# Kernel optimization log

Measured on AMD Instinct MI355X. Metric: run time of the kernel, lower is better.

The kernel has to match this reference:

```python
import jax, jax.numpy as jnp
import numpy as np

N = 100000
E = 1600000
F_IN = 512
HID = 8
HEADS = 8
NUM_CLASSES = 40
NEG_SLOPE = 0.2


def setup_inputs() -> dict:
    key = jax.random.key(0)
    ks = jax.random.split(key, 12)
    x = jax.random.normal(ks[0], (N, F_IN), dtype=jnp.float32)
    edge_index = jax.random.randint(ks[1], (2, E), 0, N, dtype=jnp.int64)
    s1 = 1.0 / np.sqrt(F_IN)
    s2 = 1.0 / np.sqrt(HID * HEADS)
    W1 = jax.random.normal(ks[2], (F_IN, HEADS * HID), dtype=jnp.float32) * s1
    a_src1 = jax.random.normal(ks[3], (HEADS, HID), dtype=jnp.float32) * s1
    a_dst1 = jax.random.normal(ks[4], (HEADS, HID), dtype=jnp.float32) * s1
    b1 = jnp.zeros((HEADS * HID,), dtype=jnp.float32)
    W2 = jax.random.normal(ks[5], (HEADS * HID, NUM_CLASSES), dtype=jnp.float32) * s2
    a_src2 = jax.random.normal(ks[6], (1, NUM_CLASSES), dtype=jnp.float32) * s2
    a_dst2 = jax.random.normal(ks[7], (1, NUM_CLASSES), dtype=jnp.float32) * s2
    b2 = jnp.zeros((NUM_CLASSES,), dtype=jnp.float32)
    return {"x": x, "edge_index": edge_index, "W1": W1, "a_src1": a_src1,
            "a_dst1": a_dst1, "b1": b1, "W2": W2, "a_src2": a_src2,
            "a_dst2": a_dst2, "b2": b2}


def _gat_conv(x, src, dst, W, a_src, a_dst, b, heads, out_ch):
    # linear projection, per-head: [N, heads, out_ch]
    h = (x @ W).reshape(N, heads, out_ch)
    # per-node attention logits [N, heads]
    al_s = jnp.einsum('nhf,hf->nh', h, a_src)
    al_d = jnp.einsum('nhf,hf->nh', h, a_dst)
    # per-edge raw scores [E', heads]
    e = jax.nn.leaky_relu(al_s[src] + al_d[dst], NEG_SLOPE)
    # segment softmax over edges sharing a destination node
    m = jax.lax.stop_gradient(jax.ops.segment_max(e, dst, num_segments=N))
    m = jnp.where(jnp.isfinite(m), m, 0.0)
    e = jnp.exp(e - m[dst])
    denom = jax.ops.segment_sum(e, dst, num_segments=N)
    alpha = e / denom[dst]  # [E', heads]
    # scatter-weighted aggregation of gathered source features
    out = jax.ops.segment_sum(alpha[:, :, None] * h[src], dst, num_segments=N)
    return out.reshape(N, heads * out_ch) + b


def reference(x, edge_index, W1, a_src1, a_dst1, b1, W2, a_src2, a_dst2, b2):
    # PyG GATConv default: add self-loops
    loops = jnp.arange(N, dtype=edge_index.dtype)
    src = jnp.concatenate([edge_index[0], loops])
    dst = jnp.concatenate([edge_index[1], loops])
    h = _gat_conv(x, src, dst, W1, a_src1, a_dst1, b1, HEADS, HID)
    h = jax.nn.elu(h)
    # dropout(p=0.6) is identity in eval mode
    out = _gat_conv(h, src, dst, W2, a_src2, a_dst2, b2, 1, NUM_CLASSES)
    return jax.nn.log_softmax(out, axis=1)
```

## Files before the change

kernel.cpp:

```cpp
#include <hip/hip_runtime.h>
#include <hip/hip_bf16.h>
#include <cstdint>
#include <cstddef>

#define N_NODES 100000
#define N_EDGES 1600000
#define E_TOT   (N_EDGES + N_NODES)
#define F_IN    512
#define HEADS   8
#define HID     8
#define F_H     64
#define NC      40
#define NEG     0.2f

#define BSH    8
#define NB     391
#define CHUNKH 8192
#define NBH    ((E_TOT + CHUNKH - 1) / CHUNKH)
#define CHUNKF 8192
#define NBF    ((E_TOT + CHUNKF - 1) / CHUNKF)
#define CAP    7168
#define GEMM_G ((N_NODES + 63) / 64)

typedef __attribute__((ext_vector_type(8))) __bf16 bf16x8;
typedef __attribute__((ext_vector_type(4))) float f32x4;
typedef __attribute__((ext_vector_type(8))) unsigned short u16x8;

__device__ __forceinline__ float bf2f(unsigned short u) {
  unsigned int w = ((unsigned int)u) << 16;
  return __builtin_bit_cast(float, w);
}
__device__ __forceinline__ unsigned short f2bf(float f) {
  __hip_bfloat16 b = __float2bfloat16(f);
  return __builtin_bit_cast(unsigned short, b);
}
__device__ __forceinline__ float lrexp(float v) {
  v = (v > 0.f) ? v : NEG * v;
  return __expf(v);
}

__device__ __forceinline__ bool detect_i64(const int* __restrict__ ei) {
  int lane = threadIdx.x & 63;
  int v = ei[2 * lane + 1];
  return __ballot(v != 0) == 0ull;
}

__device__ __forceinline__ int load_dst(const int* __restrict__ ei, bool f, int i) {
  if (i < N_EDGES) return f ? ei[2 * (N_EDGES + i)] : ei[N_EDGES + i];
  return i - N_EDGES;
}
__device__ __forceinline__ int load_src(const int* __restrict__ ei, bool f, int i) {
  if (i < N_EDGES) return f ? ei[2 * i] : ei[i];
  return i - N_EDGES;
}

__global__ __launch_bounds__(256) void k_hist_pack(
    const int* __restrict__ ei, const float* __restrict__ W1,
    uint4* __restrict__ w1f, int* __restrict__ bcnt) {
  __shared__ int h[NB];
  const int t = threadIdx.x;
  if (blockIdx.x < 16) {
    int tid = blockIdx.x * 256 + t;
    int lane = tid & 63;
    int tt = (tid >> 6) & 3;
    int s = tid >> 8;
    int k0 = s * 32 + ((lane >> 4) << 3);
    int col = tt * 16 + (lane & 15);
    u16x8 v;
#pragma unroll
    for (int i = 0; i < 8; ++i) v[i] = f2bf(W1[(size_t)(k0 + i) * F_H + col]);
    w1f[tid] = __builtin_bit_cast(uint4, v);
    return;
  }
  const int blk = blockIdx.x - 16;
  const bool f = detect_i64(ei);
  for (int i = t; i < NB; i += 256) h[i] = 0;
  __syncthreads();
  const int base = blk * CHUNKH;
#pragma unroll
  for (int j = 0; j < CHUNKH / 256; ++j) {
    int i = base + t + j * 256;
    if (i < E_TOT) atomicAdd(&h[load_dst(ei, f, i) >> BSH], 1);
  }
  __syncthreads();
  for (int i = t; i < NB; i += 256)
    if (h[i]) atomicAdd(&bcnt[i], h[i]);
}

__global__ __launch_bounds__(512) void k_bscan(const int* __restrict__ bcnt,
                                               int* __restrict__ bstart,
                                               int* __restrict__ bcur,
                                               int* __restrict__ rowstart) {
  __shared__ int sh[512];
  const int t = threadIdx.x;
  int v = (t < NB) ? bcnt[t] : 0;
  sh[t] = v;
  __syncthreads();
  for (int d = 1; d < 512; d <<= 1) {
    int u = (t >= d) ? sh[t - d] : 0;
    __syncthreads();
    sh[t] += u;
    __syncthreads();
  }
  if (t < NB) {
    int e = sh[t] - v;
    bstart[t] = e;
    bcur[t] = e;
  }
  if (t == 0) { bstart[NB] = E_TOT; rowstart[N_NODES] = E_TOT; }
}

__global__ __launch_bounds__(256) void k_bfill(const int* __restrict__ ei,
                                               int* __restrict__ bcur,
                                               unsigned int* __restrict__ inter) {
  __shared__ unsigned int ent[CHUNKF];
  __shared__ int h[NB], ofs[NB], cur[NB], gpos[NB];
  const int t = threadIdx.x;
  const int base = blockIdx.x * CHUNKF;
  const bool f = detect_i64(ei);
  for (int i = t; i < NB; i += 256) h[i] = 0;
  __syncthreads();
#pragma unroll
  for (int j = 0; j < CHUNKF / 256; ++j) {
    int i = base + t + j * 256;
    if (i < E_TOT) atomicAdd(&h[load_dst(ei, f, i) >> BSH], 1);
  }
  __syncthreads();
  if (t < 64) {
    int loc[7];
    int s = 0;
#pragma unroll
    for (int k = 0; k < 7; ++k) {
      int ix = t * 7 + k;
      int hv = (ix < NB) ? h[ix] : 0;
      loc[k] = s;
      s += hv;
    }
    int incl = s;
    for (int dd = 1; dd < 64; dd <<= 1) {
      int u = __shfl_up(incl, dd);
      if (t >= dd) incl += u;
    }
    int excl = incl - s;
#pragma unroll
    for (int k = 0; k < 7; ++k) {
      int ix = t * 7 + k;
      if (ix < NB) ofs[ix] = excl + loc[k];
    }
  }
  __syncthreads();
  for (int i = t; i < NB; i += 256) {
    cur[i] = ofs[i];
    gpos[i] = h[i] ? atomicAdd(&bcur[i], h[i]) : 0;
  }
  __syncthreads();
#pragma unroll
  for (int j = 0; j < CHUNKF / 256; ++j) {
    int i = base + t + j * 256;
    if (i < E_TOT) {
      int s = load_src(ei, f, i);
      int d = load_dst(ei, f, i);
      int p = atomicAdd(&cur[d >> BSH], 1);
      ent[p] = ((unsigned int)(d & 255) << 24) | (unsigned int)s;
    }
  }
  __syncthreads();
  const int wv = t >> 6, ln = t & 63;
  for (int b = wv; b < NB; b += 4) {
    int c = h[b];
    if (!c) continue;
    int g = gpos[b], o = ofs[b];
    for (int i = ln; i < c; i += 64) inter[g + i] = ent[o + i];
  }
}

__global__ __launch_bounds__(256) void k_gemm1g(
    const float* __restrict__ x, const uint4* __restrict__ w1f,
    const float* __restrict__ a_src, const float* __restrict__ a_dst,
    unsigned short* __restrict__ h1b, float* __restrict__ als,
    float* __restrict__ ald) {
  __shared__ float xs[2 * 64 * 64];
  const int t = threadIdx.x;
  const int lane = t & 63;
  const int wv = t >> 6;
  const int rb = blockIdx.x * 64;

  const int srow_in_kb = lane >> 4;
  const int sc16 = lane & 15;

  const int myrow = wv * 16 + (lane & 15);
  const int m7 = myrow & 7;
  const int rowbase = myrow * 64;
  const int cg2 = (lane >> 4) << 1;

  f32x4 acc[4];
#pragma unroll
  for (int i = 0; i < 4; ++i) acc[i] = (f32x4){0.f, 0.f, 0.f, 0.f};

  auto STAGE = [&](int buf, int p) {
#pragma unroll
    for (int j = 0; j < 4; ++j) {
      int kb = wv * 4 + j;
      int r = kb * 4 + srow_in_kb;
      int gr = rb + r;
      if (gr >= N_NODES) gr = N_NODES - 1;
      int c16s = sc16 ^ (r & 7);
      const float* src = x + (size_t)gr * F_IN + p * 64 + c16s * 4;
      char* dst = (char*)xs + buf * 16384 + kb * 1024;
      __builtin_amdgcn_global_load_lds(
          (const __attribute__((address_space(1))) void*)src,
          (__attribute__((address_space(3))) void*)dst, 16, 0, 0);
    }
  };

  STAGE(0, 0);
  __syncthreads();
  int buf = 0;
#pragma unroll
  for (int p = 0; p < 8; ++p) {
    if (p < 7) STAGE(buf ^ 1, p + 1);
    const float* bufp = xs + buf * 4096;
#pragma unroll
    for (int s2 = 0; s2 < 2; ++s2) {
      const int sg = p * 2 + s2;
      const int c16a = s2 * 8 + cg2;
      float4 a0 = *reinterpret_cast<const float4*>(&bufp[rowbase + ((c16a ^ m7) << 2)]);
      float4 a1 = *reinterpret_cast<const float4*>(&bufp[rowbase + (((c16a + 1) ^ m7) << 2)]);
      uint4 b0 = w1f[(sg * 4 + 0) * 64 + lane];
      uint4 b1 = w1f[(sg * 4 + 1) * 64 + lane];
      uint4 b2 = w1f[(sg * 4 + 2) * 64 + lane];
      uint4 b3 = w1f[(sg * 4 + 3) * 64 + lane];
      bf16x8 af;
      af[0] = (__bf16)a0.x; af[1] = (__bf16)a0.y;
      af[2] = (__bf16)a0.z; af[3] = (__bf16)a0.w;
      af[4] = (__bf16)a1.x; af[5] = (__bf16)a1.y;
      af[6] = (__bf16)a1.z; af[7] = (__bf16)a1.w;
      acc[0] = __builtin_amdgcn_mfma_f32_16x16x32_bf16(af, __builtin_bit_cast(bf16x8, b0), acc[0], 0, 0, 0);
      acc[1] = __builtin_amdgcn_mfma_f32_16x16x32_bf16(af, __builtin_bit_cast(bf16x8, b1), acc[1], 0, 0, 0);
      acc[2] = __builtin_amdgcn_mfma_f32_16x16x32_bf16(af, __builtin_bit_cast(bf16x8, b2), acc[2], 0, 0, 0);
      acc[3] = __builtin_amdgcn_mfma_f32_16x16x32_bf16(af, __builtin_bit_cast(bf16x8, b3), acc[3], 0, 0, 0);
    }
    __syncthreads();
    buf ^= 1;
  }

  const int r0 = rb + wv * 16 + ((lane >> 4) << 2);
  const int c = lane & 15;
#pragma unroll
  for (int tt = 0; tt < 4; ++tt) {
#pragma unroll
    for (int i = 0; i < 4; ++i) {
      int r = r0 + i;
      if (r < N_NODES) h1b[(size_t)r * F_H + tt * 16 + c] = f2bf(acc[tt][i]);
    }
  }

  float asw[4], adw[4];
#pragma unroll
  for (int tt = 0; tt < 4; ++tt) {
    asw[tt] = a_src[tt * 16 + c];
    adw[tt] = a_dst[tt * 16 + c];
  }
  float sp[4][4], dp[4][4];
#pragma unroll
  for (int tt = 0; tt < 4; ++tt)
#pragma unroll
    for (int i = 0; i < 4; ++i) {
      sp[tt][i] = acc[tt][i] * asw[tt];
      dp[tt][i] = acc[tt][i] * adw[tt];
    }
#pragma unroll
  for (int dd = 1; dd < 8; dd <<= 1)
#pragma unroll
    for (int tt = 0; tt < 4; ++tt)
#pragma unroll
      for (int i = 0; i < 4; ++i) {
        sp[tt][i] += __shfl_xor(sp[tt][i], dd);
        dp[tt][i] += __shfl_xor(dp[tt][i], dd);
      }
  if ((c & 7) == 0) {
    const int hb = c >> 3;
#pragma unroll
    for (int i = 0; i < 4; ++i) {
      int r = r0 + i;
      if (r < N_NODES) {
#pragma unroll
        for (int tt = 0; tt < 4; ++tt) {
          als[(size_t)r * HEADS + tt * 2 + hb] = sp[tt][i];
          ald[(size_t)r * HEADS + tt * 2 + hb] = dp[tt][i];
        }
      }
    }
  }
}

__global__ __launch_bounds__(256) void k_cfill(const unsigned int* __restrict__ inter,
                                               const int* __restrict__ bstart,
                                               int* __restrict__ rowstart,
                                               int* __restrict__ csrc) {
  __shared__ unsigned int out_l[CAP];
  __shared__ int cnt[256], sc[256], cur2[256];
  const int t = threadIdx.x;
  const int b = blockIdx.x;
  const int segStart = bstart[b];
  const int L = bstart[b + 1] - segStart;
  cnt[t] = 0;
  __syncthreads();
  for (int i = t; i < L; i += 256) atomicAdd(&cnt[inter[segStart + i] >> 24], 1);
  __syncthreads();
  sc[t] = cnt[t];
  __syncthreads();
  for (int d = 1; d < 256; d <<= 1) {
    int v = (t >= d) ? sc[t - d] : 0;
    __syncthreads();
    sc[t] += v;
    __syncthreads();
  }
  const int excl = sc[t] - cnt[t];
  cur2[t] = excl;
  const int node = (b << BSH) + t;
  if (node < N_NODES) rowstart[node] = segStart + excl;
  __syncthreads();
  if (L <= CAP) {
    for (int i = t; i < L; i += 256) {
      unsigned int e = inter[segStart + i];
      int p = atomicAdd(&cur2[e >> 24], 1);
      out_l[p] = e & 0xFFFFFFu;
    }
    __syncthreads();
    for (int i = t; i < L; i += 256) csrc[segStart + i] = (int)out_l[i];
  } else {
    for (int i = t; i < L; i += 256) {
      unsigned int e = inter[segStart + i];
      int p = atomicAdd(&cur2[e >> 24], 1);
      csrc[segStart + p] = (int)(e & 0xFFFFFFu);
    }
  }
}

__global__ __launch_bounds__(256) void k_agg1n(
    const int* __restrict__ rowstart, const int* __restrict__ csrc,
    const unsigned short* __restrict__ h1b, const float* __restrict__ als,
    const float* __restrict__ ald, const float* __restrict__ b1,
    unsigned short* __restrict__ hactb) {
  const int w = (int)((blockIdx.x * 256 + threadIdx.x) >> 6);
  const int lane = threadIdx.x & 63;
  const int grp = lane >> 3;
  const int l = lane & 7;
  const int n = w * 8 + grp;
  const bool live = (n < N_NODES);
  const int e0 = live ? rowstart[n] : 0;
  const int e1 = live ? rowstart[n + 1] : 0;
  const float aldv = live ? ald[(size_t)n * HEADS + l] : 0.f;

  float den = 0.f;
  float acc[8];
#pragma unroll
  for (int k = 0; k < 8; ++k) acc[k] = 0.f;

  int e = e0;
  for (; e + 4 <= e1; e += 4) {
    int4 sv = *reinterpret_cast<const int4*>(&csrc[e]);
    float a0 = als[(size_t)sv.x * HEADS + l];
    float a1 = als[(size_t)sv.y * HEADS + l];
    float a2 = als[(size_t)sv.z * HEADS + l];
    float a3 = als[(size_t)sv.w * HEADS + l];
    uint4 u0 = *reinterpret_cast<const uint4*>(&h1b[(size_t)sv.x * F_H + l * 8]);
    uint4 u1 = *reinterpret_cast<const uint4*>(&h1b[(size_t)sv.y * F_H + l * 8]);
    uint4 u2 = *reinterpret_cast<const uint4*>(&h1b[(size_t)sv.z * F_H + l * 8]);
    uint4 u3 = *reinterpret_cast<const uint4*>(&h1b[(size_t)sv.w * F_H + l * 8]);
    float p0 = lrexp(a0 + aldv), p1 = lrexp(a1 + aldv);
    float p2 = lrexp(a2 + aldv), p3 = lrexp(a3 + aldv);
    den += (p0 + p1) + (p2 + p3);
    const unsigned int* q0 = &u0.x;
    const unsigned int* q1 = &u1.x;
    const unsigned int* q2 = &u2.x;
    const unsigned int* q3 = &u3.x;
#pragma unroll
    for (int k = 0; k < 4; ++k) {
      acc[2 * k]     += p0 * bf2f((unsigned short)q0[k]) + p1 * bf2f((unsigned short)q1[k])
                      + p2 * bf2f((unsigned short)q2[k]) + p3 * bf2f((unsigned short)q3[k]);
      acc[2 * k + 1] += p0 * bf2f((unsigned short)(q0[k] >> 16)) + p1 * bf2f((unsigned short)(q1[k] >> 16))
                      + p2 * bf2f((unsigned short)(q2[k] >> 16)) + p3 * bf2f((unsigned short)(q3[k] >> 16));
    }
  }
  for (; e < e1; ++e) {
    int s = csrc[e];
    float a = als[(size_t)s * HEADS + l];
    uint4 u = *reinterpret_cast<const uint4*>(&h1b[(size_t)s * F_H + l * 8]);
    float p = lrexp(a + aldv);
    den += p;
    const unsigned int* q = &u.x;
#pragma unroll
    for (int k = 0; k < 4; ++k) {
      acc[2 * k]     += p * bf2f((unsigned short)q[k]);
      acc[2 * k + 1] += p * bf2f((unsigned short)(q[k] >> 16));
    }
  }

  if (live) {
    float inv = 1.f / den;
    uint4 outw;
    unsigned int* ow = &outw.x;
#pragma unroll
    for (int k = 0; k < 4; ++k) {
      float ox = acc[2 * k] * inv + b1[l * 8 + 2 * k];
      float oy = acc[2 * k + 1] * inv + b1[l * 8 + 2 * k + 1];
      ox = (ox > 0.f) ? ox : expm1f(ox);
      oy = (oy > 0.f) ? oy : expm1f(oy);
      ow[k] = ((unsigned int)f2bf(oy) << 16) | (unsigned int)f2bf(ox);
    }
    *reinterpret_cast<uint4*>(&hactb[(size_t)n * F_H + l * 8]) = outw;
  }
}

__global__ __launch_bounds__(256) void k_l2proj(
    const unsigned short* __restrict__ hactb, const float* __restrict__ W2,
    const float* __restrict__ a_src2, const float* __restrict__ a_dst2,
    unsigned short* __restrict__ h2b, float* __restrict__ als2,
    float* __restrict__ ald2) {
  __shared__ float hs[64 * 68];
  __shared__ float w2s[F_H * NC];
  const int t = threadIdx.x;
  const int nb = blockIdx.x * 64;
  {
    int r0 = t >> 3, c8 = t & 7;
#pragma unroll
    for (int i = 0; i < 2; ++i) {
      int r = r0 + i * 32;
      int gr = nb + r;
      u16x8 v = (u16x8)(0);
      if (gr < N_NODES)
        v = *reinterpret_cast<const u16x8*>(&hactb[(size_t)gr * F_H + c8 * 8]);
#pragma unroll
      for (int k = 0; k < 8; ++k) hs[r * 68 + c8 * 8 + k] = bf2f(v[k]);
    }
  }
  for (int i = t; i < F_H * NC; i += 256) w2s[i] = W2[i];
  __syncthreads();

  const int node = t >> 2, cg = t & 3;
  float acc[10];
#pragma unroll
  for (int c = 0; c < 10; ++c) acc[c] = 0.f;
  for (int k = 0; k < F_H; ++k) {
    float xv = hs[node * 68 + k];
#pragma unroll
    for (int c = 0; c < 10; ++c) acc[c] += xv * w2s[k * NC + cg * 10 + c];
  }
  const int gn = nb + node;
  float ps = 0.f, pd = 0.f;
#pragma unroll
  for (int c = 0; c < 10; ++c) {
    ps += acc[c] * a_src2[cg * 10 + c];
    pd += acc[c] * a_dst2[cg * 10 + c];
  }
  ps += __shfl_xor(ps, 1); ps += __shfl_xor(ps, 2);
  pd += __shfl_xor(pd, 1); pd += __shfl_xor(pd, 2);
  if (gn < N_NODES) {
#pragma unroll
    for (int c = 0; c < 10; ++c) h2b[(size_t)gn * NC + cg * 10 + c] = f2bf(acc[c]);
    if (cg == 0) { als2[gn] = ps; ald2[gn] = pd; }
  }
}

__global__ __launch_bounds__(256) void k_agg2n(
    const int* __restrict__ rowstart, const int* __restrict__ csrc,
    const unsigned short* __restrict__ h2b, const float* __restrict__ als2,
    const float* __restrict__ ald2, const float* __restrict__ b2,
    float* __restrict__ out) {
  const int w = (int)((blockIdx.x * 256 + threadIdx.x) >> 6);
  const int lane = threadIdx.x & 63;
  const int grp = lane >> 3;
  const int l = lane & 7;
  const int n = w * 8 + grp;
  const bool live = (n < N_NODES);
  const int e0 = live ? rowstart[n] : 0;
  const int e1 = live ? rowstart[n + 1] : 0;
  const float aldv = live ? ald2[n] : 0.f;
  const bool act = (l < 5);
  const int fo = act ? l * 8 : 0;

  float den = 0.f;
  float acc[8];
#pragma unroll
  for (int k = 0; k < 8; ++k) acc[k] = 0.f;

  int e = e0;
  for (; e + 4 <= e1; e += 4) {
    int4 sv = *reinterpret_cast<const int4*>(&csrc[e]);
    float a0 = als2[sv.x], a1 = als2[sv.y], a2 = als2[sv.z], a3 = als2[sv.w];
    uint4 u0 = *reinterpret_cast<const uint4*>(&h2b[(size_t)sv.x * NC + fo]);
    uint4 u1 = *reinterpret_cast<const uint4*>(&h2b[(size_t)sv.y * NC + fo]);
    uint4 u2 = *reinterpret_cast<const uint4*>(&h2b[(size_t)sv.z * NC + fo]);
    uint4 u3 = *reinterpret_cast<const uint4*>(&h2b[(size_t)sv.w * NC + fo]);
    float p0 = lrexp(a0 + aldv), p1 = lrexp(a1 + aldv);
    float p2 = lrexp(a2 + aldv), p3 = lrexp(a3 + aldv);
    den += (p0 + p1) + (p2 + p3);
    const unsigned int* q0 = &u0.x;
    const unsigned int* q1 = &u1.x;
    const unsigned int* q2 = &u2.x;
    const unsigned int* q3 = &u3.x;
#pragma unroll
    for (int k = 0; k < 4; ++k) {
      acc[2 * k]     += p0 * bf2f((unsigned short)q0[k]) + p1 * bf2f((unsigned short)q1[k])
                      + p2 * bf2f((unsigned short)q2[k]) + p3 * bf2f((unsigned short)q3[k]);
      acc[2 * k + 1] += p0 * bf2f((unsigned short)(q0[k] >> 16)) + p1 * bf2f((unsigned short)(q1[k] >> 16))
                      + p2 * bf2f((unsigned short)(q2[k] >> 16)) + p3 * bf2f((unsigned short)(q3[k] >> 16));
    }
  }
  for (; e < e1; ++e) {
    int s = csrc[e];
    float a = als2[s];
    uint4 u = *reinterpret_cast<const uint4*>(&h2b[(size_t)s * NC + fo]);
    float p = lrexp(a + aldv);
    den += p;
    const unsigned int* q = &u.x;
#pragma unroll
    for (int k = 0; k < 4; ++k) {
      acc[2 * k]     += p * bf2f((unsigned short)q[k]);
      acc[2 * k + 1] += p * bf2f((unsigned short)(q[k] >> 16));
    }
  }

  float o[8];
  float inv = 1.f / den;
  float mx = -1e30f;
#pragma unroll
  for (int k = 0; k < 8; ++k) {
    o[k] = act ? (acc[k] * inv + b2[fo + k]) : -1e30f;
    mx = fmaxf(mx, o[k]);
  }
  mx = fmaxf(mx, __shfl_xor(mx, 1));
  mx = fmaxf(mx, __shfl_xor(mx, 2));
  mx = fmaxf(mx, __shfl_xor(mx, 4));
  float se = 0.f;
#pragma unroll
  for (int k = 0; k < 8; ++k) se += act ? __expf(o[k] - mx) : 0.f;
  se += __shfl_xor(se, 1);
  se += __shfl_xor(se, 2);
  se += __shfl_xor(se, 4);
  if (live && act) {
    float ls = __logf(se);
    float4 r0, r1;
    r0.x = o[0] - mx - ls; r0.y = o[1] - mx - ls;
    r0.z = o[2] - mx - ls; r0.w = o[3] - mx - ls;
    r1.x = o[4] - mx - ls; r1.y = o[5] - mx - ls;
    r1.z = o[6] - mx - ls; r1.w = o[7] - mx - ls;
    *reinterpret_cast<float4*>(&out[(size_t)n * NC + l * 8]) = r0;
    *reinterpret_cast<float4*>(&out[(size_t)n * NC + l * 8 + 4]) = r1;
  }
}

extern "C" void kernel_launch(void* const* d_in, const int* in_sizes, int n_in,
                              void* d_out, int out_size, void* d_ws, size_t ws_size,
                              hipStream_t stream) {
  const float* x      = (const float*)d_in[0];
  const int*   ei     = (const int*)d_in[1];
  const float* W1     = (const float*)d_in[2];
  const float* a_src1 = (const float*)d_in[3];
  const float* a_dst1 = (const float*)d_in[4];
  const float* b1     = (const float*)d_in[5];
  const float* W2     = (const float*)d_in[6];
  const float* a_src2 = (const float*)d_in[7];
  const float* a_dst2 = (const float*)d_in[8];
  const float* b2     = (const float*)d_in[9];
  float* out = (float*)d_out;

  char* ws = (char*)d_ws;
  size_t o = 0;
  auto carve = [&](size_t bytes) -> char* {
    char* p = ws + o;
    o = (o + bytes + 255) & ~(size_t)255;
    return p;
  };
  int*   bcnt     = (int*)carve((size_t)NB * 4);
  int*   bstart   = (int*)carve((size_t)(NB + 1) * 4);
  int*   bcur     = (int*)carve((size_t)NB * 4);
  int*   rowstart = (int*)carve((size_t)(N_NODES + 1) * 4);
  unsigned int* inter = (unsigned int*)carve((size_t)E_TOT * 4);
  int*   csrc     = (int*)carve((size_t)(E_TOT + 8) * 4);
  uint4* w1f      = (uint4*)carve((size_t)4096 * 16);
  unsigned short* h1b   = (unsigned short*)carve((size_t)N_NODES * F_H * 2);
  float* als1     = (float*)carve((size_t)N_NODES * HEADS * 4);
  float* ald1     = (float*)carve((size_t)N_NODES * HEADS * 4);
  unsigned short* hactb = (unsigned short*)carve((size_t)N_NODES * F_H * 2);
  unsigned short* h2b   = (unsigned short*)carve((size_t)(N_NODES * NC + 8) * 2);
  float* als2     = (float*)carve((size_t)N_NODES * 4);
  float* ald2     = (float*)carve((size_t)N_NODES * 4);
  (void)ws_size; (void)n_in; (void)in_sizes; (void)out_size;

  hipMemsetAsync(bcnt, 0, (size_t)NB * 4, stream);
  k_hist_pack<<<16 + NBH, 256, 0, stream>>>(ei, W1, w1f, bcnt);
  k_bscan<<<1, 512, 0, stream>>>(bcnt, bstart, bcur, rowstart);
  k_bfill<<<NBF, 256, 0, stream>>>(ei, bcur, inter);
  k_gemm1g<<<GEMM_G, 256, 0, stream>>>(x, w1f, a_src1, a_dst1, h1b, als1, ald1);
  k_cfill<<<NB, 256, 0, stream>>>(inter, bstart, rowstart, csrc);

  const int aggGrid = (N_NODES + 31) / 32;
  k_agg1n<<<aggGrid, 256, 0, stream>>>(rowstart, csrc, h1b, als1, ald1, b1, hactb);
  k_l2proj<<<(N_NODES + 63) / 64, 256, 0, stream>>>(hactb, W2, a_src2, a_dst2, h2b, als2, ald2);
  k_agg2n<<<aggGrid, 256, 0, stream>>>(rowstart, csrc, h2b, als2, ald2, b2, out);
}
```

Measured before the change: 255.3 us.

## Restructure layer-1 GEMM to stage full 16-row chunks with per-wave column tiles

The x@W1 GEMM kernel now stages 16 complete rows of x (all 512 features) per step, four chunks per 64-row block, instead of 64-wide K slices of all 64 rows. Each wave owns a 16-column output tile, one head pair, and loops over the full K with a single accumulator. The XOR swizzle on LDS is dropped. This aims to make global loads contiguous per row and cut accumulator registers, but risks LDS bank conflicts on the unswizzled A reads and loads each B fragment once per row chunk, more often than before.

New measurement: 376.6 us. 47.5% more time.

```diff
diff --git a/kernel.cpp b/kernel.cpp
--- a/kernel.cpp
+++ b/kernel.cpp
@@ -174,123 +174,92 @@
   }
 }
 
-__global__ __launch_bounds__(256) void k_gemm1g(
+__global__ __launch_bounds__(256) void k_gemm1r(
     const float* __restrict__ x, const uint4* __restrict__ w1f,
     const float* __restrict__ a_src, const float* __restrict__ a_dst,
     unsigned short* __restrict__ h1b, float* __restrict__ als,
     float* __restrict__ ald) {
-  __shared__ float xs[2 * 64 * 64];
+  __shared__ float xs[2][16 * 512];
   const int t = threadIdx.x;
   const int lane = t & 63;
   const int wv = t >> 6;
   const int rb = blockIdx.x * 64;
 
-  const int srow_in_kb = lane >> 4;
-  const int sc16 = lane & 15;
-
-  const int myrow = wv * 16 + (lane & 15);
-  const int m7 = myrow & 7;
-  const int rowbase = myrow * 64;
-  const int cg2 = (lane >> 4) << 1;
-
-  f32x4 acc[4];
-#pragma unroll
-  for (int i = 0; i < 4; ++i) acc[i] = (f32x4){0.f, 0.f, 0.f, 0.f};
-
-  auto STAGE = [&](int buf, int p) {
+  const int arow = lane & 15;
+  const int koct = (lane >> 4) << 3;
+  const int gcol = wv * 16 + (lane & 15);
+  const float asw = a_src[gcol];
+  const float adw = a_dst[gcol];
+  const int ghead = (gcol >> 3);
+  const int lr0 = (lane >> 4) << 2;
+
+  auto STAGE = [&](int buf, int c) {
 #pragma unroll
     for (int j = 0; j < 4; ++j) {
-      int kb = wv * 4 + j;
-      int r = kb * 4 + srow_in_kb;
-      int gr = rb + r;
+      int r = wv * 4 + j;
+      int gr = rb + c * 16 + r;
       if (gr >= N_NODES) gr = N_NODES - 1;
-      int c16s = sc16 ^ (r & 7);
-      const float* src = x + (size_t)gr * F_IN + p * 64 + c16s * 4;
-      char* dst = (char*)xs + buf * 16384 + kb * 1024;
-      __builtin_amdgcn_global_load_lds(
-          (const __attribute__((address_space(1))) void*)src,
-          (__attribute__((address_space(3))) void*)dst, 16, 0, 0);
+#pragma unroll
+      for (int hh = 0; hh < 2; ++hh) {
+        const float* src = x + (size_t)gr * F_IN + hh * 256 + lane * 4;
+        char* dst = (char*)&xs[buf][r * 512 + hh * 256];
+        __builtin_amdgcn_global_load_lds(
+            (const __attribute__((address_space(1))) void*)src,
+            (__attribute__((address_space(3))) void*)dst, 16, 0, 0);
+      }
     }
   };
 
   STAGE(0, 0);
-  __syncthreads();
   int buf = 0;
 #pragma unroll
-  for (int p = 0; p < 8; ++p) {
-    if (p < 7) STAGE(buf ^ 1, p + 1);
-    const float* bufp = xs + buf * 4096;
-#pragma unroll
-    for (int s2 = 0; s2 < 2; ++s2) {
-      const int sg = p * 2 + s2;
-      const int c16a = s2 * 8 + cg2;
-      float4 a0 = *reinterpret_cast<const float4*>(&bufp[rowbase + ((c16a ^ m7) << 2)]);
-      float4 a1 = *reinterpret_cast<const float4*>(&bufp[rowbase + (((c16a + 1) ^ m7) << 2)]);
-      uint4 b0 = w1f[(sg * 4 + 0) * 64 + lane];
-      uint4 b1 = w1f[(sg * 4 + 1) * 64 + lane];
-      uint4 b2 = w1f[(sg * 4 + 2) * 64 + lane];
-      uint4 b3 = w1f[(sg * 4 + 3) * 64 + lane];
+  for (int c = 0; c < 4; ++c) {
+    if (c < 3) STAGE(buf ^ 1, c + 1);
+    __syncthreads();
+    const float* bufp = xs[buf];
+
+    f32x4 acc = (f32x4){0.f, 0.f, 0.f, 0.f};
+#pragma unroll
+    for (int sg = 0; sg < 16; ++sg) {
+      const float* ap = &bufp[arow * 512 + sg * 32 + koct];
+      float4 a0 = *reinterpret_cast<const float4*>(ap);
+      float4 a1 = *reinterpret_cast<const float4*>(ap + 4);
+      uint4 b = w1f[(sg * 4 + wv) * 64 + lane];
       bf16x8 af;
       af[0] = (__bf16)a0.x; af[1] = (__bf16)a0.y;
       af[2] = (__bf16)a0.z; af[3] = (__bf16)a0.w;
       af[4] = (__bf16)a1.x; af[5] = (__bf16)a1.y;
       af[6] = (__bf16)a1.z; af[7] = (__bf16)a1.w;
-      acc[0] = __builtin_amdgcn_mfma_f32_16x16x32_bf16(af, __builtin_bit_cast(bf16x8, b0), acc[0], 0, 0, 0);
-      acc[1] = __builtin_amdgcn_mfma_f32_16x16x32_bf16(af, __builtin_bit_cast(bf16x8, b1), acc[1], 0, 0, 0);
-      acc[2] = __builtin_amdgcn_mfma_f32_16x16x32_bf16(af, __builtin_bit_cast(bf16x8, b2), acc[2], 0, 0, 0);
-      acc[3] = __builtin_amdgcn_mfma_f32_16x16x32_bf16(af, __builtin_bit_cast(bf16x8, b3), acc[3], 0, 0, 0);
-    }
-    __syncthreads();
-    buf ^= 1;
-  }
-
-  const int r0 = rb + wv * 16 + ((lane >> 4) << 2);
-  const int c = lane & 15;
-#pragma unroll
-  for (int tt = 0; tt < 4; ++tt) {
+      acc = __builtin_amdgcn_mfma_f32_16x16x32_bf16(af, __builtin_bit_cast(bf16x8, b), acc, 0, 0, 0);
+    }
+
+    float sp[4], dp[4];
 #pragma unroll
     for (int i = 0; i < 4; ++i) {
-      int r = r0 + i;
-      if (r < N_NODES) h1b[(size_t)r * F_H + tt * 16 + c] = f2bf(acc[tt][i]);
-    }
-  }
-
-  float asw[4], adw[4];
-#pragma unroll
-  for (int tt = 0; tt < 4; ++tt) {
-    asw[tt] = a_src[tt * 16 + c];
-    adw[tt] = a_dst[tt * 16 + c];
-  }
-  float sp[4][4], dp[4][4];
-#pragma unroll
-  for (int tt = 0; tt < 4; ++tt)
-#pragma unroll
-    for (int i = 0; i < 4; ++i) {
-      sp[tt][i] = acc[tt][i] * asw[tt];
-      dp[tt][i] = acc[tt][i] * adw[tt];
-    }
-#pragma unroll
-  for (int dd = 1; dd < 8; dd <<= 1)
-#pragma unroll
-    for (int tt = 0; tt < 4; ++tt)
+      int grow = rb + c * 16 + lr0 + i;
+      if (grow < N_NODES) h1b[(size_t)grow * F_H + gcol] = f2bf(acc[i]);
+      sp[i] = acc[i] * asw;
+      dp[i] = acc[i] * adw;
+    }
+#pragma unroll
+    for (int dd = 1; dd < 8; dd <<= 1)
 #pragma unroll
       for (int i = 0; i < 4; ++i) {
-        sp[tt][i] += __shfl_xor(sp[tt][i], dd);
-        dp[tt][i] += __shfl_xor(dp[tt][i], dd);
+        sp[i] += __shfl_xor(sp[i], dd);
+        dp[i] += __shfl_xor(dp[i], dd);
       }
-  if ((c & 7) == 0) {
-    const int hb = c >> 3;
-#pragma unroll
-    for (int i = 0; i < 4; ++i) {
-      int r = r0 + i;
-      if (r < N_NODES) {
-#pragma unroll
-        for (int tt = 0; tt < 4; ++tt) {
-          als[(size_t)r * HEADS + tt * 2 + hb] = sp[tt][i];
-          ald[(size_t)r * HEADS + tt * 2 + hb] = dp[tt][i];
+    if ((lane & 7) == 0) {
+#pragma unroll
+      for (int i = 0; i < 4; ++i) {
+        int grow = rb + c * 16 + lr0 + i;
+        if (grow < N_NODES) {
+          als[(size_t)grow * HEADS + ghead] = sp[i];
+          ald[(size_t)grow * HEADS + ghead] = dp[i];
         }
       }
     }
+    __syncthreads();
+    buf ^= 1;
   }
 }
 
@@ -594,7 +563,7 @@
   k_hist_pack<<<16 + NBH, 256, 0, stream>>>(ei, W1, w1f, bcnt);
   k_bscan<<<1, 512, 0, stream>>>(bcnt, bstart, bcur, rowstart);
   k_bfill<<<NBF, 256, 0, stream>>>(ei, bcur, inter);
-  k_gemm1g<<<GEMM_G, 256, 0, stream>>>(x, w1f, a_src1, a_dst1, h1b, als1, ald1);
+  k_gemm1r<<<GEMM_G, 256, 0, stream>>>(x, w1f, a_src1, a_dst1, h1b, als1, ald1);
   k_cfill<<<NB, 256, 0, stream>>>(inter, bstart, rowstart, csrc);
 
   const int aggGrid = (N_NODES + 31) / 32;
```
